# Kernel tuning notes

Measured on AMD Instinct MI355X. Metric: run time of the kernel, lower is better.

The kernel has to match this reference:

```python
import jax, jax.numpy as jnp
import numpy as np

DIM, H, HD, S, K = 2560, 40, 64, 64, 4  # dim, n_heads, head_dim, state_dim, conv kernel
EPS = 1e-5


def _layer_norm(x, g, b):
    m = jnp.mean(x, axis=-1, keepdims=True)
    v = jnp.mean((x - m) ** 2, axis=-1, keepdims=True)
    return (x - m) * jax.lax.rsqrt(v + EPS) * g + b


def setup_inputs() -> dict:
    key = jax.random.key(0)
    ks = jax.random.split(key, 10)
    w = lambda k, shape: jax.random.normal(k, shape, jnp.float32) * 0.02
    return {
        "x": jax.random.normal(ks[0], (2, 2048, DIM), jnp.float32),
        "W_r": w(ks[1], (DIM, DIM)),
        "W_k": w(ks[2], (DIM, DIM)),
        "W_v": w(ks[3], (DIM, DIM)),
        "W_g": w(ks[4], (DIM, DIM)),
        "W_xproj": w(ks[5], (H * 3 * S, DIM)),
        "W_dt": w(ks[6], (DIM, H * S)),
        "b_dt": jnp.ones((DIM,), jnp.float32),  # dt_proj bias init to 1.0
        "conv_w": w(ks[7], (DIM, 1, K)),  # depthwise conv (out=DIM, in/groups=1, k)
        "ln1_g": jnp.ones((DIM,), jnp.float32),
        "ln1_b": jnp.zeros((DIM,), jnp.float32),
        "ln2_g": jnp.ones((DIM,), jnp.float32),
        "ln2_b": jnp.zeros((DIM,), jnp.float32),
        "W_out": w(ks[8], (DIM, DIM)),
    }


def reference(x, W_r, W_k, W_v, W_g, W_xproj, W_dt, b_dt, conv_w,
              ln1_g, ln1_b, ln2_g, ln2_b, W_out):
    B, L, D = x.shape
    # causal depthwise conv: torch Conv1d(pad=3)[:, :L] == left-pad by K-1
    xc = jax.lax.conv_general_dilated(
        x.transpose(0, 2, 1), conv_w, window_strides=(1,), padding=[(K - 1, 0)],
        feature_group_count=D, dimension_numbers=("NCH", "OIH", "NCH"),
    ).transpose(0, 2, 1)
    x = _layer_norm(x + xc, ln1_g, ln1_b)

    proj = (x @ W_xproj.T).reshape(B, L, H, 3 * S)
    dt_raw, B_vec, C_vec = jnp.split(proj, 3, axis=-1)  # each (B,L,H,S)
    dt = jax.nn.softplus(dt_raw.reshape(B, L, H * S) @ W_dt.T + b_dt)
    w = jnp.exp(-dt).reshape(B, L, H, S)

    r = jax.nn.sigmoid(x @ W_r.T).reshape(B, L, H, HD)
    k = (x @ W_k.T).reshape(B, L, H, HD)
    v = (x @ W_v.T).reshape(B, L, H, HD)
    g = jax.nn.sigmoid(x @ W_g.T).reshape(B, L, H, HD)
    kv = k * v  # (B,L,H,HD)

    def step(state, inp):
        w_t, B_t, C_t, kv_t, r_t, g_t = inp
        # state: (B,H,S,HD); decay per state row, rank-1 B ⊗ (k*v) update
        state = w_t[..., None] * state + B_t[..., None] * kv_t[:, :, None, :]
        y = jnp.einsum("bhsd,bhs->bhd", state, C_t)
        return state, r_t * y * g_t

    seq = tuple(jnp.moveaxis(a, 1, 0) for a in (w, B_vec, C_vec, kv, r, g))
    state0 = jnp.zeros((B, H, S, HD), x.dtype)
    final_state, outs = jax.lax.scan(step, state0, seq)  # outs: (L,B,H,HD)
    out = jnp.moveaxis(outs, 0, 1).reshape(B, L, D)
    out = _layer_norm(x + out @ W_out.T, ln2_g, ln2_b)
    return out, final_state
```

## Files before the change

kernel.cpp:

```cpp
#include <hip/hip_runtime.h>
#include <cstddef>
#include <cstdint>

#define DIM 2560
#define NH 40
#define HDD 64
#define SD 64
#define KC 4
#define BB 2
#define LL 2048
#define MTOT (BB*LL)
#define NPROJ (NH*3*SD)
#define NC 16
#define CH (LL/NC)
#define BH (BB*NH)

typedef unsigned short u16;
typedef __attribute__((ext_vector_type(8))) short bf16x8;
typedef __attribute__((ext_vector_type(4))) float f32x4;

__device__ inline float bf2f(u16 u) { return __uint_as_float(((unsigned)u) << 16); }
__device__ inline float bflo(unsigned u) { return __uint_as_float(u << 16); }
__device__ inline float bfhi(unsigned u) { return __uint_as_float(u & 0xffff0000u); }
__device__ inline u16 f2bf(float f) {
  unsigned x = __float_as_uint(f);
  unsigned r = (x + 0x7fffu + ((x >> 16) & 1u)) >> 16;
  return (u16)r;
}

__device__ inline void gload16(const void* g, void* lds) {
  __builtin_amdgcn_global_load_lds(
      (const __attribute__((address_space(1))) void*)g,
      (__attribute__((address_space(3))) void*)(uint32_t)(size_t)lds,
      16, 0, 0);
}

__global__ __launch_bounds__(256) void cvt_kernel(
    const float* __restrict__ src, u16* __restrict__ dst, int n4) {
  int i = blockIdx.x * 256 + threadIdx.x;
  int stride = gridDim.x * 256;
  for (; i < n4; i += stride) {
    float4 v = *(const float4*)(src + (size_t)i * 4);
    ushort4 o;
    o.x = f2bf(v.x); o.y = f2bf(v.y); o.z = f2bf(v.z); o.w = f2bf(v.w);
    *(ushort4*)(dst + (size_t)i * 4) = o;
  }
}

struct Cvt4Args { const float* s0; const float* s1; const float* s2; const float* s3;
                  u16* d0; u16* d1; u16* d2; u16* d3; };
__global__ __launch_bounds__(256) void cvt4_kernel(Cvt4Args a, int n4each) {
  int i = blockIdx.x * 256 + threadIdx.x;
  int stride = gridDim.x * 256;
  int total = 4 * n4each;
  for (; i < total; i += stride) {
    int which = i / n4each;
    int loc = i - which * n4each;
    const float* s = (which == 0) ? a.s0 : (which == 1) ? a.s1 : (which == 2) ? a.s2 : a.s3;
    u16* d = (which == 0) ? a.d0 : (which == 1) ? a.d1 : (which == 2) ? a.d2 : a.d3;
    float4 v = *(const float4*)(s + (size_t)loc * 4);
    ushort4 o;
    o.x = f2bf(v.x); o.y = f2bf(v.y); o.z = f2bf(v.z); o.w = f2bf(v.w);
    *(ushort4*)(d + (size_t)loc * 4) = o;
  }
}

__global__ __launch_bounds__(256) void fill_kernel(float* p, int n, float v) {
  int i = blockIdx.x * 256 + threadIdx.x;
  if (i < n) p[i] = v;
}

__device__ inline void block_reduce2(float& sum, float& sq, float* red) {
  #pragma unroll
  for (int off = 32; off; off >>= 1) {
    sum += __shfl_down(sum, off, 64);
    sq  += __shfl_down(sq,  off, 64);
  }
  int wid = threadIdx.x >> 6, lane = threadIdx.x & 63;
  if (lane == 0) { red[wid*2] = sum; red[wid*2+1] = sq; }
  __syncthreads();
  sum = red[0] + red[2] + red[4] + red[6];
  sq  = red[1] + red[3] + red[5] + red[7];
}

__global__ __launch_bounds__(256) void conv_ln1_kernel(
    const float* __restrict__ x, const float* __restrict__ cw,
    const float* __restrict__ g1, const float* __restrict__ b1,
    u16* __restrict__ x1) {
  __shared__ float red[8];
  int bl = blockIdx.x;
  int l  = bl & (LL - 1);
  int t  = threadIdx.x;
  const float* xr = x + (size_t)bl * DIM;
  float vals[10];
  float sum = 0.f, sq = 0.f;
  #pragma unroll
  for (int i = 0; i < 10; ++i) {
    int d = t + 256 * i;
    float acc = xr[d];
    #pragma unroll
    for (int j = 0; j < KC; ++j) {
      int ll = l - (KC - 1) + j;
      if (ll >= 0) acc += x[(size_t)(bl - l + ll) * DIM + d] * cw[d * KC + j];
    }
    vals[i] = acc; sum += acc; sq += acc * acc;
  }
  block_reduce2(sum, sq, red);
  float mean = sum * (1.f / DIM);
  float var  = sq * (1.f / DIM) - mean * mean;
  float rstd = rsqrtf(var + 1e-5f);
  u16* orow = x1 + (size_t)bl * DIM;
  #pragma unroll
  for (int i = 0; i < 10; ++i) {
    int d = t + 256 * i;
    orow[d] = f2bf((vals[i] - mean) * rstd * g1[d] + b1[d]);
  }
}

__global__ __launch_bounds__(256) void ln2_kernel(
    const u16* __restrict__ x1, const u16* __restrict__ y2,
    const float* __restrict__ g2, const float* __restrict__ b2,
    float* __restrict__ out) {
  __shared__ float red[8];
  int bl = blockIdx.x;
  int t  = threadIdx.x;
  const u16* ar = x1 + (size_t)bl * DIM;
  const u16* br = y2 + (size_t)bl * DIM;
  float vals[10];
  float sum = 0.f, sq = 0.f;
  #pragma unroll
  for (int i = 0; i < 10; ++i) {
    int d = t + 256 * i;
    float v = bf2f(ar[d]) + bf2f(br[d]);
    vals[i] = v; sum += v; sq += v * v;
  }
  block_reduce2(sum, sq, red);
  float mean = sum * (1.f / DIM);
  float var  = sq * (1.f / DIM) - mean * mean;
  float rstd = rsqrtf(var + 1e-5f);
  float* orow = out + (size_t)bl * DIM;
  #pragma unroll
  for (int i = 0; i < 10; ++i) {
    int d = t + 256 * i;
    orow[d] = (vals[i] - mean) * rstd * g2[d] + b2[d];
  }
}

#define GEMM_PIPE_LOOP(STAGEM) \
  STAGEM(0, 0); \
  STAGEM(1, 32); \
  { \
    int nt = K / 32; \
    for (int tt = 0; tt < nt; ++tt) { \
      if (tt == nt - 1) { asm volatile("s_waitcnt vmcnt(0)" ::: "memory"); } \
      else              { asm volatile("s_waitcnt vmcnt(4)" ::: "memory"); } \
      __builtin_amdgcn_sched_barrier(0); \
      __builtin_amdgcn_s_barrier(); \
      __builtin_amdgcn_sched_barrier(0); \
      int buf = tt & 1; \
      bf16x8 a[4], b[4]; \
      _Pragma("unroll") \
      for (int i = 0; i < 4; ++i) a[i] = *(const bf16x8*)(rA + buf * 4096 + i * 16 * 32); \
      _Pragma("unroll") \
      for (int j = 0; j < 4; ++j) b[j] = *(const bf16x8*)(rB + buf * 4096 + j * 16 * 32); \
      __builtin_amdgcn_s_setprio(1); \
      _Pragma("unroll") \
      for (int i = 0; i < 4; ++i) \
        _Pragma("unroll") \
        for (int j = 0; j < 4; ++j) \
          acc[i][j] = __builtin_amdgcn_mfma_f32_16x16x32_bf16(a[i], b[j], acc[i][j], 0, 0, 0); \
      __builtin_amdgcn_s_setprio(0); \
      __builtin_amdgcn_sched_barrier(0); \
      __builtin_amdgcn_s_barrier(); \
      __builtin_amdgcn_sched_barrier(0); \
      if (tt + 2 < nt) { int k2 = (tt + 2) * 32; STAGEM(buf, k2); } \
    } \
  }

template<int EPI, bool REMAP>
__global__ __launch_bounds__(256) void gemm_mfma(
    const u16* __restrict__ A, int lda,
    const u16* __restrict__ Wb,
    const float* __restrict__ bias,
    u16* __restrict__ C1, int ldc,
    int K) {
  __shared__ u16 As[2 * 128 * 32];
  __shared__ u16 Bs[2 * 128 * 32];
  int t = threadIdx.x;
  int w = t >> 6, l = t & 63;
  int wr = w >> 1, wc = w & 1;
  int m0 = blockIdx.y * 128;
  int n0 = blockIdx.x * 128;

  f32x4 acc[4][4];
  #pragma unroll
  for (int i = 0; i < 4; ++i)
    #pragma unroll
    for (int j = 0; j < 4; ++j)
      acc[i][j] = (f32x4){0.f, 0.f, 0.f, 0.f};

  int srow = 32 * w + (l >> 2);
  int scol = (l & 3) * 8;
  const u16* gA = A  + (size_t)(m0 + srow) * lda + scol;
  const u16* gB = Wb + (size_t)(n0 + srow) * K   + scol;
  int ldsOff = (32 * w) * 32;

  int fr = l & 15;
  int kc = (l >> 4) * 8;
  const u16* rA = As + (size_t)(wr * 64 + fr) * 32 + kc;
  const u16* rB = Bs + (size_t)(wc * 64 + fr) * 32 + kc;

#define STAGE_S(buf, k0) do { \
    gload16(gA + (k0), As + (buf) * 4096 + ldsOff); \
    gload16(gA + (size_t)16 * lda + (k0), As + (buf) * 4096 + ldsOff + 16 * 32); \
    gload16(gB + (k0), Bs + (buf) * 4096 + ldsOff); \
    gload16(gB + (size_t)16 * K + (k0), Bs + (buf) * 4096 + ldsOff + 16 * 32); } while (0)

  GEMM_PIPE_LOOP(STAGE_S)
#undef STAGE_S

  int crow = (l >> 4) * 4;
  int ccol = l & 15;
  #pragma unroll
  for (int j = 0; j < 4; ++j) {
    int col = n0 + wc * 64 + j * 16 + ccol;
    int colr = col;
    if (REMAP) {
      int h = col / 192, r3 = col % 192;
      colr = (r3 / 64) * 2560 + h * 64 + (r3 & 63);
    }
    float bv = (EPI == 2) ? bias[col] : 0.f;
    #pragma unroll
    for (int i = 0; i < 4; ++i) {
      #pragma unroll
      for (int q = 0; q < 4; ++q) {
        int row = m0 + wr * 64 + i * 16 + crow + q;
        float v = acc[i][j][q];
        if constexpr (EPI == 2) v = 1.f / (1.f + expf(v + bv));
        C1[(size_t)row * ldc + colr] = f2bf(v);
      }
    }
  }
}

__global__ __launch_bounds__(256) void gemm_big4(
    const u16* __restrict__ A,
    const u16* __restrict__ W0, const u16* __restrict__ W1,
    const u16* __restrict__ W2, const u16* __restrict__ W3,
    u16* __restrict__ C0, u16* __restrict__ C1b,
    u16* __restrict__ C2, u16* __restrict__ C3,
    int K) {
  __shared__ u16 As[2 * 128 * 32];
  __shared__ u16 Bs[2 * 128 * 32];
  int t = threadIdx.x;
  int w = t >> 6, l = t & 63;
  int wr = w >> 1, wc = w & 1;
  int m0 = blockIdx.y * 128;
  int n0g = blockIdx.x * 128;
  int which = n0g / 2560;
  int n0 = n0g - which * 2560;
  const u16* Wsel = (which == 0) ? W0 : (which == 1) ? W1 : (which == 2) ? W2 : W3;
  u16* Csel = (which == 0) ? C0 : (which == 1) ? C1b : (which == 2) ? C2 : C3;
  bool sig = (which < 2);

  f32x4 acc[4][4];
  #pragma unroll
  for (int i = 0; i < 4; ++i)
    #pragma unroll
    for (int j = 0; j < 4; ++j)
      acc[i][j] = (f32x4){0.f, 0.f, 0.f, 0.f};

  int srow = 32 * w + (l >> 2);
  int scol = (l & 3) * 8;
  const u16* gA = A    + (size_t)(m0 + srow) * K + scol;
  const u16* gB = Wsel + (size_t)(n0 + srow) * K + scol;
  int ldsOff = (32 * w) * 32;

  int fr = l & 15;
  int kc = (l >> 4) * 8;
  const u16* rA = As + (size_t)(wr * 64 + fr) * 32 + kc;
  const u16* rB = Bs + (size_t)(wc * 64 + fr) * 32 + kc;

#define STAGE_B(buf, k0) do { \
    gload16(gA + (k0), As + (buf) * 4096 + ldsOff); \
    gload16(gA + (size_t)16 * K + (k0), As + (buf) * 4096 + ldsOff + 16 * 32); \
    gload16(gB + (k0), Bs + (buf) * 4096 + ldsOff); \
    gload16(gB + (size_t)16 * K + (k0), Bs + (buf) * 4096 + ldsOff + 16 * 32); } while (0)

  GEMM_PIPE_LOOP(STAGE_B)
#undef STAGE_B

  int crow = (l >> 4) * 4;
  int ccol = l & 15;
  #pragma unroll
  for (int j = 0; j < 4; ++j) {
    int col = n0 + wc * 64 + j * 16 + ccol;
    #pragma unroll
    for (int i = 0; i < 4; ++i) {
      #pragma unroll
      for (int q = 0; q < 4; ++q) {
        int row = m0 + wr * 64 + i * 16 + crow + q;
        float v = acc[i][j][q];
        if (sig) v = 1.f / (1.f + expf(-v));
        Csel[(size_t)row * DIM + col] = f2bf(v);
      }
    }
  }
}

__global__ __launch_bounds__(128) void scan_local_kernel(
    const u16* __restrict__ wdec, const u16* __restrict__ proj,
    const u16* __restrict__ kb, const u16* __restrict__ vb,
    u16* __restrict__ yout,
    float* __restrict__ Sbuf, float* __restrict__ Pbuf) {
  int bx = blockIdx.x;
  int bh = bx / NC, c = bx % NC;
  int b = bh / NH, h = bh % NH;
  int wv = threadIdx.x >> 6;
  int lane = threadIdx.x & 63;
  int sg = lane >> 3, dd = lane & 7;
  int s0 = sg * 8;
  int d0 = wv * 32 + dd * 4;
  int l0 = c * CH;

  const u16* fw = wdec + ((size_t)(b * LL + l0)) * DIM + h * 64 + s0;
  const u16* fB = proj + ((size_t)(b * LL + l0)) * NPROJ + 2560 + h * 64 + s0;
  const u16* fC = fB + 2560;
  const u16* fk = kb + ((size_t)(b * LL + l0)) * DIM + h * 64 + d0;
  const u16* fv = vb + ((size_t)(b * LL + l0)) * DIM + h * 64 + d0;
  u16* py = yout + ((size_t)(b * LL + l0)) * NPROJ + h * 64 + d0;

  float st[8][4];
  float pc[8];
  #pragma unroll
  for (int i = 0; i < 8; ++i) {
    pc[i] = 1.f;
    #pragma unroll
    for (int j = 0; j < 4; ++j) st[i][j] = 0.f;
  }

#define P1_DECL(n) uint4 wS##n, BS##n, CS##n; uint2 kS##n, vS##n
#define P1_LOAD(n) do { \
    wS##n = *(const uint4*)fw; BS##n = *(const uint4*)fB; \
    CS##n = *(const uint4*)fC; kS##n = *(const uint2*)fk; \
    vS##n = *(const uint2*)fv; \
    fw += DIM; fB += NPROJ; fC += NPROJ; fk += DIM; fv += DIM; } while (0)
#define P1_PROC(n) do { \
    float wv8[8], Bv[8], Cv[8], kv4[4], pr[4]; \
    wv8[0]=bflo(wS##n.x); wv8[1]=bfhi(wS##n.x); wv8[2]=bflo(wS##n.y); wv8[3]=bfhi(wS##n.y); \
    wv8[4]=bflo(wS##n.z); wv8[5]=bfhi(wS##n.z); wv8[6]=bflo(wS##n.w); wv8[7]=bfhi(wS##n.w); \
    Bv[0]=bflo(BS##n.x); Bv[1]=bfhi(BS##n.x); Bv[2]=bflo(BS##n.y); Bv[3]=bfhi(BS##n.y); \
    Bv[4]=bflo(BS##n.z); Bv[5]=bfhi(BS##n.z); Bv[6]=bflo(BS##n.w); Bv[7]=bfhi(BS##n.w); \
    Cv[0]=bflo(CS##n.x); Cv[1]=bfhi(CS##n.x); Cv[2]=bflo(CS##n.y); Cv[3]=bfhi(CS##n.y); \
    Cv[4]=bflo(CS##n.z); Cv[5]=bfhi(CS##n.z); Cv[6]=bflo(CS##n.w); Cv[7]=bfhi(CS##n.w); \
    kv4[0]=bflo(kS##n.x)*bflo(vS##n.x); kv4[1]=bfhi(kS##n.x)*bfhi(vS##n.x); \
    kv4[2]=bflo(kS##n.y)*bflo(vS##n.y); kv4[3]=bfhi(kS##n.y)*bfhi(vS##n.y); \
    pr[0]=0.f; pr[1]=0.f; pr[2]=0.f; pr[3]=0.f; \
    _Pragma("unroll") \
    for (int i = 0; i < 8; ++i) { \
      pc[i] *= wv8[i]; \
      _Pragma("unroll") \
      for (int j = 0; j < 4; ++j) { \
        st[i][j] = fmaf(wv8[i], st[i][j], Bv[i] * kv4[j]); \
        pr[j] = fmaf(st[i][j], Cv[i], pr[j]); } } \
    _Pragma("unroll") \
    for (int j = 0; j < 4; ++j) { \
      pr[j] += __shfl_xor(pr[j], 8, 64); \
      pr[j] += __shfl_xor(pr[j], 16, 64); \
      pr[j] += __shfl_xor(pr[j], 32, 64); } \
    if (lane < 8) { \
      uint2 ov; \
      ov.x = (unsigned)f2bf(pr[0]) | ((unsigned)f2bf(pr[1]) << 16); \
      ov.y = (unsigned)f2bf(pr[2]) | ((unsigned)f2bf(pr[3]) << 16); \
      *(uint2*)py = ov; } \
    py += NPROJ; } while (0)

  P1_DECL(0); P1_DECL(1); P1_DECL(2); P1_DECL(3);
  P1_LOAD(0); P1_LOAD(1); P1_LOAD(2); P1_LOAD(3);
  for (int l = 0; l < CH; l += 4) {
    P1_PROC(0); P1_LOAD(0);
    P1_PROC(1); P1_LOAD(1);
    P1_PROC(2); P1_LOAD(2);
    P1_PROC(3); P1_LOAD(3);
  }
#undef P1_DECL
#undef P1_LOAD
#undef P1_PROC

  float* Sp = Sbuf + (((size_t)c * BH + bh) * 64 + s0) * 64 + d0;
  #pragma unroll
  for (int i = 0; i < 8; ++i) {
    float4 v; v.x = st[i][0]; v.y = st[i][1]; v.z = st[i][2]; v.w = st[i][3];
    *(float4*)(Sp + (size_t)i * 64) = v;
  }
  if (wv == 0 && dd == 0) {
    #pragma unroll
    for (int i = 0; i < 8; ++i)
      Pbuf[((size_t)c * BH + bh) * 64 + s0 + i] = pc[i];
  }
}

__global__ __launch_bounds__(256) void scan_combine_kernel(
    float* __restrict__ Sbuf, const float* __restrict__ Pbuf,
    float* __restrict__ fstate) {
  int bh = blockIdx.x;
  int t = threadIdx.x;
  int s = t >> 2, j0 = (t & 3) * 16;
  float stin[16];
  #pragma unroll
  for (int k = 0; k < 16; ++k) stin[k] = 0.f;
  for (int c = 0; c < NC; ++c) {
    float* Sp = Sbuf + (((size_t)c * BH + bh) * 64 + s) * 64 + j0;
    float Pc = Pbuf[((size_t)c * BH + bh) * 64 + s];
    #pragma unroll
    for (int q = 0; q < 4; ++q) {
      float4 a = *(const float4*)(Sp + q * 4);
      float4 cur;
      cur.x = stin[q*4+0]; cur.y = stin[q*4+1];
      cur.z = stin[q*4+2]; cur.w = stin[q*4+3];
      *(float4*)(Sp + q * 4) = cur;
      stin[q*4+0] = a.x + Pc * stin[q*4+0];
      stin[q*4+1] = a.y + Pc * stin[q*4+1];
      stin[q*4+2] = a.z + Pc * stin[q*4+2];
      stin[q*4+3] = a.w + Pc * stin[q*4+3];
    }
  }
  float* fp = fstate + ((size_t)bh * 64 + s) * 64 + j0;
  #pragma unroll
  for (int q = 0; q < 4; ++q) {
    float4 v;
    v.x = stin[q*4+0]; v.y = stin[q*4+1];
    v.z = stin[q*4+2]; v.w = stin[q*4+3];
    *(float4*)(fp + q * 4) = v;
  }
}

__global__ __launch_bounds__(128) void scan_correct_kernel(
    const u16* __restrict__ wdec, const u16* __restrict__ proj,
    const u16* __restrict__ rb, const u16* __restrict__ gb,
    const float* __restrict__ Sbuf, u16* __restrict__ yio) {
  int bx = blockIdx.x;
  int bh = bx / NC, c = bx % NC;
  int b = bh / NH, h = bh % NH;
  int wv = threadIdx.x >> 6;
  int lane = threadIdx.x & 63;
  int sg = lane >> 3, dd = lane & 7;
  int s0 = sg * 8;
  int d0 = wv * 32 + dd * 4;
  int l0 = c * CH;

  const float* Sp = Sbuf + (((size_t)c * BH + bh) * 64 + s0) * 64 + d0;
  float stin[8][4];
  #pragma unroll
  for (int i = 0; i < 8; ++i) {
    float4 v = *(const float4*)(Sp + (size_t)i * 64);
    stin[i][0] = v.x; stin[i][1] = v.y; stin[i][2] = v.z; stin[i][3] = v.w;
  }

  const u16* fw = wdec + ((size_t)(b * LL + l0)) * DIM + h * 64 + s0;
  const u16* fC = proj + ((size_t)(b * LL + l0)) * NPROJ + 5120 + h * 64 + s0;
  const u16* fy = yio  + ((size_t)(b * LL + l0)) * NPROJ + h * 64 + d0;
  const u16* fr2 = rb + ((size_t)(b * LL + l0)) * DIM + h * 64 + d0;
  const u16* fg2 = gb + ((size_t)(b * LL + l0)) * DIM + h * 64 + d0;
  u16* py = yio + ((size_t)(b * LL + l0)) * NPROJ + h * 64 + d0;

  float pc[8];
  #pragma unroll
  for (int i = 0; i < 8; ++i) pc[i] = 1.f;

#define P3_DECL(n) uint4 wT##n, CT##n; uint2 yT##n, rT##n, gT##n
#define P3_LOAD(n) do { \
    wT##n = *(const uint4*)fw; CT##n = *(const uint4*)fC; \
    yT##n = *(const uint2*)fy; rT##n = *(const uint2*)fr2; gT##n = *(const uint2*)fg2; \
    fw += DIM; fC += NPROJ; fy += NPROJ; fr2 += DIM; fg2 += DIM; } while (0)
#define P3_PROC(n) do { \
    float wv8[8], Cv[8], ac[8], pr[4]; \
    wv8[0]=bflo(wT##n.x); wv8[1]=bfhi(wT##n.x); wv8[2]=bflo(wT##n.y); wv8[3]=bfhi(wT##n.y); \
    wv8[4]=bflo(wT##n.z); wv8[5]=bfhi(wT##n.z); wv8[6]=bflo(wT##n.w); wv8[7]=bfhi(wT##n.w); \
    Cv[0]=bflo(CT##n.x); Cv[1]=bfhi(CT##n.x); Cv[2]=bflo(CT##n.y); Cv[3]=bfhi(CT##n.y); \
    Cv[4]=bflo(CT##n.z); Cv[5]=bfhi(CT##n.z); Cv[6]=bflo(CT##n.w); Cv[7]=bfhi(CT##n.w); \
    pr[0]=0.f; pr[1]=0.f; pr[2]=0.f; pr[3]=0.f; \
    _Pragma("unroll") \
    for (int i = 0; i < 8; ++i) { \
      pc[i] *= wv8[i]; ac[i] = pc[i] * Cv[i]; \
      _Pragma("unroll") \
      for (int j = 0; j < 4; ++j) pr[j] = fmaf(ac[i], stin[i][j], pr[j]); } \
    _Pragma("unroll") \
    for (int j = 0; j < 4; ++j) { \
      pr[j] += __shfl_xor(pr[j], 8, 64); \
      pr[j] += __shfl_xor(pr[j], 16, 64); \
      pr[j] += __shfl_xor(pr[j], 32, 64); } \
    if (lane < 8) { \
      float y0 = (bflo(yT##n.x) + pr[0]) * bflo(rT##n.x) * bflo(gT##n.x); \
      float y1 = (bfhi(yT##n.x) + pr[1]) * bfhi(rT##n.x) * bfhi(gT##n.x); \
      float y2 = (bflo(yT##n.y) + pr[2]) * bflo(rT##n.y) * bflo(gT##n.y); \
      float y3 = (bfhi(yT##n.y) + pr[3]) * bfhi(rT##n.y) * bfhi(gT##n.y); \
      uint2 ov; \
      ov.x = (unsigned)f2bf(y0) | ((unsigned)f2bf(y1) << 16); \
      ov.y = (unsigned)f2bf(y2) | ((unsigned)f2bf(y3) << 16); \
      *(uint2*)py = ov; } \
    py += NPROJ; } while (0)

  P3_DECL(0); P3_DECL(1); P3_DECL(2); P3_DECL(3);
  P3_LOAD(0); P3_LOAD(1); P3_LOAD(2); P3_LOAD(3);
  for (int l = 0; l < CH; l += 4) {
    P3_PROC(0); P3_LOAD(0);
    P3_PROC(1); P3_LOAD(1);
    P3_PROC(2); P3_LOAD(2);
    P3_PROC(3); P3_LOAD(3);
  }
#undef P3_DECL
#undef P3_LOAD
#undef P3_PROC
}

extern "C" void kernel_launch(void* const* d_in, const int* in_sizes, int n_in,
                              void* d_out, int out_size, void* d_ws, size_t ws_size,
                              hipStream_t stream) {
  const float* x    = (const float*)d_in[0];
  const float* W_r  = (const float*)d_in[1];
  const float* W_k  = (const float*)d_in[2];
  const float* W_v  = (const float*)d_in[3];
  const float* W_g  = (const float*)d_in[4];
  const float* W_xp = (const float*)d_in[5];
  const float* W_dt = (const float*)d_in[6];
  const float* b_dt = (const float*)d_in[7];
  const float* cw   = (const float*)d_in[8];
  const float* ln1g = (const float*)d_in[9];
  const float* ln1b = (const float*)d_in[10];
  const float* ln2g = (const float*)d_in[11];
  const float* ln2b = (const float*)d_in[12];
  const float* W_o  = (const float*)d_in[13];

  float* out    = (float*)d_out;
  float* fstate = out + (size_t)MTOT * DIM;

  const size_t nBL = (size_t)MTOT * DIM;
  const size_t nPJ = (size_t)MTOT * NPROJ;
  const size_t nWX = (size_t)NPROJ * DIM;
  const size_t nDD = (size_t)DIM * DIM;
  const size_t needed = (nBL * 5 + nPJ + nWX) * sizeof(u16);
  if (ws_size < needed) {
    fill_kernel<<<(out_size + 255) / 256, 256, 0, stream>>>(out, out_size, 1234.5f);
    return;
  }

  u16* wsp  = (u16*)d_ws;
  u16* x1   = wsp;
  u16* proj = x1 + nBL;
  u16* wdec = proj + nPJ;
  u16* rb   = wdec + nBL;
  u16* gb   = rb + nBL;
  u16* kvb  = gb + nBL;
  u16* wscr = kvb + nBL;
  float* Sbuf = (float*)wscr;
  float* Pbuf = Sbuf + (size_t)NC * BH * 64 * 64;

  u16* vscr = (u16*)d_out;
  u16* wvb  = vscr + nBL;

  const int nDD4 = (int)(nDD / 4);

  conv_ln1_kernel<<<MTOT, 256, 0, stream>>>(x, cw, ln1g, ln1b, x1);

  cvt_kernel<<<2048, 256, 0, stream>>>(W_xp, wscr, NPROJ * DIM / 4);
  gemm_mfma<0,true ><<<dim3(NPROJ/128, MTOT/128), 256, 0, stream>>>(x1, DIM, wscr, nullptr, proj, NPROJ, DIM);

  cvt_kernel<<<2048, 256, 0, stream>>>(W_dt, wscr, nDD4);
  gemm_mfma<2,false><<<dim3(DIM/128, MTOT/128), 256, 0, stream>>>(proj, NPROJ, wscr, b_dt, wdec, DIM, DIM);

  Cvt4Args ca;
  ca.s0 = W_r; ca.s1 = W_g; ca.s2 = W_k; ca.s3 = W_v;
  ca.d0 = wscr; ca.d1 = wscr + nDD; ca.d2 = wscr + 2 * nDD; ca.d3 = wvb;
  cvt4_kernel<<<2048, 256, 0, stream>>>(ca, nDD4);
  gemm_big4<<<dim3(4 * DIM / 128, MTOT / 128), 256, 0, stream>>>(
      x1, wscr, wscr + nDD, wscr + 2 * nDD, wvb, rb, gb, kvb, vscr, DIM);

  scan_local_kernel<<<BH * NC, 128, 0, stream>>>(wdec, proj, kvb, vscr, proj, Sbuf, Pbuf);
  scan_combine_kernel<<<BH, 256, 0, stream>>>(Sbuf, Pbuf, fstate);
  scan_correct_kernel<<<BH * NC, 128, 0, stream>>>(wdec, proj, rb, gb, Sbuf, proj);

  cvt_kernel<<<2048, 256, 0, stream>>>(W_o, wscr, nDD4);
  gemm_mfma<0,false><<<dim3(DIM/128, MTOT/128), 256, 0, stream>>>(proj, NPROJ, wscr, nullptr, wdec, DIM, DIM);

  ln2_kernel<<<MTOT, 256, 0, stream>>>(x1, wdec, ln2g, ln2b, out);
}
```

Before: 987.7 us.

## Replace 128x128 GEMMs with 256x256-tile 8-wave pipelined MFMA kernel

Introduces a templated gemm256 kernel with 256x256 output tiles, 512 threads, an XOR-swizzled LDS layout and a hand-scheduled double-buffered pipeline. The pipeline interleaves global loads with MFMA phases using explicit vmcnt waits, barriers and setprio. It replaces both the x-projection GEMM and the fused four-way r/g/k/v GEMM. The intent is more data reuse per tile, fewer LDS bank conflicts and better load/compute overlap in the dominant GEMMs. In exchange it uses 128 KB of LDS per block and large accumulator register use, and the larger tiles mean fewer blocks, which risks poor occupancy and wave-quantization on the smaller GEMM.

Result: faster. 895.7 us (-9.3%).

```diff
diff --git a/kernel.cpp b/kernel.cpp
--- a/kernel.cpp
+++ b/kernel.cpp
@@ -243,66 +243,150 @@
   }
 }
 
-__global__ __launch_bounds__(256) void gemm_big4(
+template<int MODE>
+__global__ __launch_bounds__(512) void gemm256(
     const u16* __restrict__ A,
     const u16* __restrict__ W0, const u16* __restrict__ W1,
     const u16* __restrict__ W2, const u16* __restrict__ W3,
     u16* __restrict__ C0, u16* __restrict__ C1b,
-    u16* __restrict__ C2, u16* __restrict__ C3,
-    int K) {
-  __shared__ u16 As[2 * 128 * 32];
-  __shared__ u16 Bs[2 * 128 * 32];
-  int t = threadIdx.x;
-  int w = t >> 6, l = t & 63;
-  int wr = w >> 1, wc = w & 1;
-  int m0 = blockIdx.y * 128;
-  int n0g = blockIdx.x * 128;
-  int which = n0g / 2560;
-  int n0 = n0g - which * 2560;
-  const u16* Wsel = (which == 0) ? W0 : (which == 1) ? W1 : (which == 2) ? W2 : W3;
-  u16* Csel = (which == 0) ? C0 : (which == 1) ? C1b : (which == 2) ? C2 : C3;
-  bool sig = (which < 2);
-
-  f32x4 acc[4][4];
-  #pragma unroll
-  for (int i = 0; i < 4; ++i)
+    u16* __restrict__ C2, u16* __restrict__ C3) {
+  const int K = 2560;
+  __shared__ u16 As[32768];
+  __shared__ u16 Bs[32768];
+  int tid = threadIdx.x;
+  int wid = tid >> 6, l = tid & 63;
+  int wr = wid >> 2, wc = wid & 3;
+  int m0 = blockIdx.y * 256;
+  int n0g = blockIdx.x * 256;
+  int which = (MODE == 1) ? (n0g / 2560) : 0;
+  int n0 = (MODE == 1) ? (n0g - which * 2560) : n0g;
+  const u16* Wsel = (MODE == 0) ? W0 :
+                    ((which == 0) ? W0 : (which == 1) ? W1 : (which == 2) ? W2 : W3);
+  u16* Csel = (MODE == 0) ? C0 :
+              ((which == 0) ? C0 : (which == 1) ? C1b : (which == 2) ? C2 : C3);
+
+  f32x4 acc[8][4];
+  #pragma unroll
+  for (int i = 0; i < 8; ++i)
     #pragma unroll
     for (int j = 0; j < 4; ++j)
       acc[i][j] = (f32x4){0.f, 0.f, 0.f, 0.f};
 
-  int srow = 32 * w + (l >> 2);
-  int scol = (l & 3) * 8;
-  const u16* gA = A    + (size_t)(m0 + srow) * K + scol;
-  const u16* gB = Wsel + (size_t)(n0 + srow) * K + scol;
-  int ldsOff = (32 * w) * 32;
-
-  int fr = l & 15;
-  int kc = (l >> 4) * 8;
-  const u16* rA = As + (size_t)(wr * 64 + fr) * 32 + kc;
-  const u16* rB = Bs + (size_t)(wc * 64 + fr) * 32 + kc;
-
-#define STAGE_B(buf, k0) do { \
-    gload16(gA + (k0), As + (buf) * 4096 + ldsOff); \
-    gload16(gA + (size_t)16 * K + (k0), As + (buf) * 4096 + ldsOff + 16 * 32); \
-    gload16(gB + (k0), Bs + (buf) * 4096 + ldsOff); \
-    gload16(gB + (size_t)16 * K + (k0), Bs + (buf) * 4096 + ldsOff + 16 * 32); } while (0)
-
-  GEMM_PIPE_LOOP(STAGE_B)
-#undef STAGE_B
-
-  int crow = (l >> 4) * 4;
-  int ccol = l & 15;
+  int swzc = (((tid & 3) ^ ((tid >> 3) & 3)) * 8);
+  const u16* sA = A    + (size_t)(m0 + (tid >> 2)) * K + swzc;
+  const u16* sB = Wsel + (size_t)(n0 + (tid >> 2)) * K + swzc;
+
+  int fr = l & 15, u = l >> 4;
+  int rsw = ((u ^ ((fr >> 1) & 3)) * 8);
+  const u16* rA0 = As + (size_t)(wr * 128 + fr) * 32 + rsw;
+  const u16* rB0 = Bs + (size_t)(wc * 64 + fr) * 32 + rsw;
+
+#define STGA(buf, ks, T) do { \
+    const u16* _s = sA + (size_t)(T) * 64 + (ks) * 32; \
+    u16* _d = As + (buf) * 16384 + (ks) * 8192 + tid * 8; \
+    gload16(_s, _d); gload16(_s + (size_t)128 * K, _d + 4096); } while (0)
+#define STGB(buf, ks, T) do { \
+    const u16* _s = sB + (size_t)(T) * 64 + (ks) * 32; \
+    u16* _d = Bs + (buf) * 16384 + (ks) * 8192 + tid * 8; \
+    gload16(_s, _d); gload16(_s + (size_t)128 * K, _d + 4096); } while (0)
+#define RDA(i, buf, ks) (*(const bf16x8*)(rA0 + (buf) * 16384 + (ks) * 8192 + (i) * 512))
+#define RDB(j, buf, ks) (*(const bf16x8*)(rB0 + (buf) * 16384 + (ks) * 8192 + (j) * 512))
+#define CLOSEB do { \
+    __builtin_amdgcn_sched_barrier(0); \
+    __builtin_amdgcn_s_barrier(); \
+    __builtin_amdgcn_sched_barrier(0); } while (0)
+#define VM8 asm volatile("s_waitcnt vmcnt(8)" ::: "memory")
+#define VM4 asm volatile("s_waitcnt vmcnt(4)" ::: "memory")
+#define VM0 asm volatile("s_waitcnt vmcnt(0)" ::: "memory")
+#define MFMA16(mh) do { \
+    acc[(mh)*4+0][0] = __builtin_amdgcn_mfma_f32_16x16x32_bf16(a0, b0, acc[(mh)*4+0][0], 0, 0, 0); \
+    acc[(mh)*4+0][1] = __builtin_amdgcn_mfma_f32_16x16x32_bf16(a0, b1, acc[(mh)*4+0][1], 0, 0, 0); \
+    acc[(mh)*4+0][2] = __builtin_amdgcn_mfma_f32_16x16x32_bf16(a0, b2, acc[(mh)*4+0][2], 0, 0, 0); \
+    acc[(mh)*4+0][3] = __builtin_amdgcn_mfma_f32_16x16x32_bf16(a0, b3, acc[(mh)*4+0][3], 0, 0, 0); \
+    acc[(mh)*4+1][0] = __builtin_amdgcn_mfma_f32_16x16x32_bf16(a1, b0, acc[(mh)*4+1][0], 0, 0, 0); \
+    acc[(mh)*4+1][1] = __builtin_amdgcn_mfma_f32_16x16x32_bf16(a1, b1, acc[(mh)*4+1][1], 0, 0, 0); \
+    acc[(mh)*4+1][2] = __builtin_amdgcn_mfma_f32_16x16x32_bf16(a1, b2, acc[(mh)*4+1][2], 0, 0, 0); \
+    acc[(mh)*4+1][3] = __builtin_amdgcn_mfma_f32_16x16x32_bf16(a1, b3, acc[(mh)*4+1][3], 0, 0, 0); \
+    acc[(mh)*4+2][0] = __builtin_amdgcn_mfma_f32_16x16x32_bf16(a2, b0, acc[(mh)*4+2][0], 0, 0, 0); \
+    acc[(mh)*4+2][1] = __builtin_amdgcn_mfma_f32_16x16x32_bf16(a2, b1, acc[(mh)*4+2][1], 0, 0, 0); \
+    acc[(mh)*4+2][2] = __builtin_amdgcn_mfma_f32_16x16x32_bf16(a2, b2, acc[(mh)*4+2][2], 0, 0, 0); \
+    acc[(mh)*4+2][3] = __builtin_amdgcn_mfma_f32_16x16x32_bf16(a2, b3, acc[(mh)*4+2][3], 0, 0, 0); \
+    acc[(mh)*4+3][0] = __builtin_amdgcn_mfma_f32_16x16x32_bf16(a3, b0, acc[(mh)*4+3][0], 0, 0, 0); \
+    acc[(mh)*4+3][1] = __builtin_amdgcn_mfma_f32_16x16x32_bf16(a3, b1, acc[(mh)*4+3][1], 0, 0, 0); \
+    acc[(mh)*4+3][2] = __builtin_amdgcn_mfma_f32_16x16x32_bf16(a3, b2, acc[(mh)*4+3][2], 0, 0, 0); \
+    acc[(mh)*4+3][3] = __builtin_amdgcn_mfma_f32_16x16x32_bf16(a3, b3, acc[(mh)*4+3][3], 0, 0, 0); } while (0)
+#define PHASE(buf, ks, mh, RB, STG_STMT) do { \
+    if (RB) { b0 = RDB(0, buf, ks); b1 = RDB(1, buf, ks); \
+              b2 = RDB(2, buf, ks); b3 = RDB(3, buf, ks); } \
+    a0 = RDA((mh)*4+0, buf, ks); a1 = RDA((mh)*4+1, buf, ks); \
+    a2 = RDA((mh)*4+2, buf, ks); a3 = RDA((mh)*4+3, buf, ks); \
+    STG_STMT; \
+    __builtin_amdgcn_sched_barrier(0); \
+    __builtin_amdgcn_s_barrier(); \
+    __builtin_amdgcn_sched_barrier(0); \
+    __builtin_amdgcn_s_setprio(1); \
+    MFMA16(mh); \
+    __builtin_amdgcn_s_setprio(0); } while (0)
+
+  bf16x8 a0, a1, a2, a3, b0, b1, b2, b3;
+
+  STGA(0, 0, 0); STGB(0, 0, 0);
+  STGA(0, 1, 0); STGB(0, 1, 0);
+  STGA(1, 0, 1); STGB(1, 0, 1);
+  VM8; CLOSEB;
+
+  const int nIter = 20;
+  for (int it = 0; it < nIter - 1; ++it) {
+    int T1 = 2 * it + 1, T2 = 2 * it + 2, T3 = 2 * it + 3;
+    PHASE(0, 0, 0, 1, STGA(1, 1, T1));            CLOSEB;
+    PHASE(0, 0, 1, 0, STGB(1, 1, T1));  VM8;      CLOSEB;
+    PHASE(0, 1, 0, 1, STGA(0, 0, T2));            CLOSEB;
+    PHASE(0, 1, 1, 0, STGB(0, 0, T2));  VM8;      CLOSEB;
+    PHASE(1, 0, 0, 1, STGA(0, 1, T2));            CLOSEB;
+    PHASE(1, 0, 1, 0, STGB(0, 1, T2));  VM8;      CLOSEB;
+    PHASE(1, 1, 0, 1, STGA(1, 0, T3));            CLOSEB;
+    PHASE(1, 1, 1, 0, STGB(1, 0, T3));  VM8;      CLOSEB;
+  }
+  {
+    int T1 = 2 * (nIter - 1) + 1;
+    PHASE(0, 0, 0, 1, STGA(1, 1, T1));            CLOSEB;
+    PHASE(0, 0, 1, 0, STGB(1, 1, T1));  VM8;      CLOSEB;
+    PHASE(0, 1, 0, 1, (void)0);                   CLOSEB;
+    PHASE(0, 1, 1, 0, (void)0);         VM4;      CLOSEB;
+    PHASE(1, 0, 0, 1, (void)0);                   CLOSEB;
+    PHASE(1, 0, 1, 0, (void)0);         VM0;      CLOSEB;
+    PHASE(1, 1, 0, 1, (void)0);                   CLOSEB;
+    PHASE(1, 1, 1, 0, (void)0);                   CLOSEB;
+  }
+#undef STGA
+#undef STGB
+#undef RDA
+#undef RDB
+#undef CLOSEB
+#undef VM8
+#undef VM4
+#undef VM0
+#undef MFMA16
+#undef PHASE
+
+  bool sig = (MODE == 1) && (which < 2);
+  int ldc = (MODE == 0) ? NPROJ : DIM;
   #pragma unroll
   for (int j = 0; j < 4; ++j) {
-    int col = n0 + wc * 64 + j * 16 + ccol;
-    #pragma unroll
-    for (int i = 0; i < 4; ++i) {
+    int col = n0 + wc * 64 + j * 16 + fr;
+    int colr = col;
+    if (MODE == 0) {
+      int h = col / 192, r3 = col % 192;
+      colr = (r3 / 64) * 2560 + h * 64 + (r3 & 63);
+    }
+    #pragma unroll
+    for (int i = 0; i < 8; ++i) {
       #pragma unroll
       for (int q = 0; q < 4; ++q) {
-        int row = m0 + wr * 64 + i * 16 + crow + q;
+        int row = m0 + wr * 128 + i * 16 + u * 4 + q;
         float v = acc[i][j][q];
         if (sig) v = 1.f / (1.f + expf(-v));
-        Csel[(size_t)row * DIM + col] = f2bf(v);
+        Csel[(size_t)row * ldc + colr] = f2bf(v);
       }
     }
   }
@@ -564,7 +648,8 @@
   conv_ln1_kernel<<<MTOT, 256, 0, stream>>>(x, cw, ln1g, ln1b, x1);
 
   cvt_kernel<<<2048, 256, 0, stream>>>(W_xp, wscr, NPROJ * DIM / 4);
-  gemm_mfma<0,true ><<<dim3(NPROJ/128, MTOT/128), 256, 0, stream>>>(x1, DIM, wscr, nullptr, proj, NPROJ, DIM);
+  gemm256<0><<<dim3(NPROJ/256, MTOT/256), 512, 0, stream>>>(
+      x1, wscr, nullptr, nullptr, nullptr, proj, nullptr, nullptr, nullptr);
 
   cvt_kernel<<<2048, 256, 0, stream>>>(W_dt, wscr, nDD4);
   gemm_mfma<2,false><<<dim3(DIM/128, MTOT/128), 256, 0, stream>>>(proj, NPROJ, wscr, b_dt, wdec, DIM, DIM);
@@ -573,8 +658,8 @@
   ca.s0 = W_r; ca.s1 = W_g; ca.s2 = W_k; ca.s3 = W_v;
   ca.d0 = wscr; ca.d1 = wscr + nDD; ca.d2 = wscr + 2 * nDD; ca.d3 = wvb;
   cvt4_kernel<<<2048, 256, 0, stream>>>(ca, nDD4);
-  gemm_big4<<<dim3(4 * DIM / 128, MTOT / 128), 256, 0, stream>>>(
-      x1, wscr, wscr + nDD, wscr + 2 * nDD, wvb, rb, gb, kvb, vscr, DIM);
+  gemm256<1><<<dim3(4 * DIM / 256, MTOT / 256), 512, 0, stream>>>(
+      x1, wscr, wscr + nDD, wscr + 2 * nDD, wvb, rb, gb, kvb, vscr);
 
   scan_local_kernel<<<BH * NC, 128, 0, stream>>>(wdec, proj, kvb, vscr, proj, Sbuf, Pbuf);
   scan_combine_kernel<<<BH, 256, 0, stream>>>(Sbuf, Pbuf, fstate);
```
